# Performance work log

Hardware: AMD Instinct MI355X
Metric: run time of the kernel (lower is better)

Reference implementation:

```python
import jax, jax.numpy as jnp
import numpy as np

N_BUS = 2000
BATCH = 512
N_EDGES = 3072000
SN_MVA = 100.0
ALPHA = 0.9
PHYS_SCALE = 0.02
DEG2RAD = np.pi / 180.0


def setup_inputs() -> dict:
    key = jax.random.key(0)
    ks = jax.random.split(key, 13)
    N = BATCH * N_BUS
    return {
        "y_pred": jax.random.normal(ks[0], (BATCH, N_BUS * 2), jnp.float32),
        "y_true": jax.random.normal(ks[1], (BATCH, N_BUS * 2), jnp.float32),
        "x_input": jax.random.normal(ks[2], (N, 7), jnp.float32),
        "edge_index": jax.random.randint(ks[3], (2, N_EDGES), 0, N),
        "edge_attr": jax.random.normal(ks[4], (N_EDGES, 4), jnp.float32),
        "x_mean": jax.random.normal(ks[5], (N_BUS, 7), jnp.float32),
        "x_std": jax.random.uniform(ks[6], (N_BUS, 7), jnp.float32, 0.5, 1.5),
        "y_mean": jax.random.normal(ks[7], (N_BUS, 2), jnp.float32),
        "y_std": jax.random.uniform(ks[8], (N_BUS, 2), jnp.float32, 0.5, 1.5),
        "edge_mean": jax.random.normal(ks[9], (4,), jnp.float32),
        "edge_std": jax.random.uniform(ks[10], (4,), jnp.float32, 0.5, 1.5),
        "load_bus_mask": jax.random.bernoulli(ks[11], 0.8, (N_BUS,)),
        "bus_shunt_pu": jax.random.normal(ks[12], (N_BUS, 2), jnp.float32) * 0.01,
    }


def reference(y_pred, y_true, x_input, edge_index, edge_attr,
              x_mean, x_std, y_mean, y_std, edge_mean, edge_std,
              load_bus_mask, bus_shunt_pu):
    B, n = BATCH, N_BUS
    N = B * n
    # --- MSE in denormalised target space ---
    yp = y_pred.reshape(B, n, 2) * y_std + y_mean   # [B, n, 2] (Vm, Va_deg)
    yt = y_true.reshape(B, n, 2) * y_std + y_mean
    mse = jnp.mean((yp - yt) ** 2)
    # --- denormalise node features ---
    x_pq = (x_input.reshape(B, n, 7)[:, :, :2] * x_std[:, :2] + x_mean[:, :2])
    x_pq = x_pq.reshape(N, 2) / SN_MVA              # per-unit P, Q demand
    x_phys = jnp.concatenate([yp.reshape(N, 2), x_pq], axis=-1)  # [N,4] Vm,Va,P,Q
    edge_pu = edge_attr * edge_std + edge_mean      # [E,4] Gs,Bs,Gm,Bm
    # --- per-edge power-flow message (flow='target_to_source': i=row0, j=row1) ---
    src, dst = edge_index[0], edge_index[1]
    xi = x_phys[src]
    xj = x_phys[dst]
    vm_i, va_i = xi[:, 0], xi[:, 1] * DEG2RAD
    vm_j, va_j = xj[:, 0], xj[:, 1] * DEG2RAD
    e_i, f_i = vm_i * jnp.cos(va_i), vm_i * jnp.sin(va_i)
    e_j, f_j = vm_j * jnp.cos(va_j), vm_j * jnp.sin(va_j)
    Gs, Bs, Gm, Bm = edge_pu[:, 0], edge_pu[:, 1], edge_pu[:, 2], edge_pu[:, 3]
    I_re = Gs * e_i - Bs * f_i + Gm * e_j - Bm * f_j
    I_im = Gs * f_i + Bs * e_i + Gm * f_j + Bm * e_j
    Pji = -(e_i * I_re + f_i * I_im)
    Qji = -(f_i * I_re - e_i * I_im)
    msg = jnp.stack([Pji, Qji], axis=-1)            # [E,2]
    # --- scatter-add aggregation into source nodes ---
    agg = jax.ops.segment_sum(msg, src, num_segments=N)  # [N,2]
    # --- KCL residual per node ---
    vm_sq = x_phys[:, 0] ** 2
    shunt = jnp.tile(bus_shunt_pu, (B, 1))          # [N,2]
    dP = -agg[:, 0] + x_phys[:, 2] + vm_sq * shunt[:, 0]
    dQ = -agg[:, 1] + x_phys[:, 3] - vm_sq * shunt[:, 1]
    sq = dP ** 2 + dQ ** 2                          # [N]
    w = jnp.tile(load_bus_mask, B).astype(sq.dtype)
    phys = jnp.sum(sq * w) / jnp.sum(w)             # masked mean
    return ALPHA * mse + (1.0 - ALPHA) * PHYS_SCALE * phys
```

## Files before the change

kernel.cpp:

```cpp
#include <hip/hip_runtime.h>
#include <hip/hip_bf16.h>
#include <hip/hip_fp16.h>

#define N_BUS   2000
#define BATCH   512
#define NNODES  (BATCH * N_BUS)
#define NEDGES  3072000

constexpr float SN_INV     = 0.01f;
constexpr float ALPHA_C    = 0.9f;
constexpr float PHYS_SCALE = 0.02f;
constexpr float DEG2RAD_C  = 0.017453292519943295f;

typedef float v4f __attribute__((ext_vector_type(4)));

__device__ __forceinline__ void atomic_pk_add_h2(__half2* addr, float P, float Q) {
    __half2 v = __floats2half2_rn(P, Q);
#if __has_builtin(__builtin_amdgcn_global_atomic_fadd_v2f16)
    typedef _Float16 v2h __attribute__((ext_vector_type(2)));
    __builtin_amdgcn_global_atomic_fadd_v2f16(
        (__attribute__((address_space(1))) v2h*)(void*)addr,
        *reinterpret_cast<v2h*>(&v));
#else
    unsafeAtomicAdd(addr, v);
#endif
}

__device__ __forceinline__ float wave_reduce(float v) {
    #pragma unroll
    for (int off = 32; off > 0; off >>= 1) v += __shfl_down(v, off, 64);
    return v;
}

__global__ __launch_bounds__(256) void node_prep(
    const float* __restrict__ y_pred, const float* __restrict__ y_true,
    const float* __restrict__ x_input,
    const float* __restrict__ x_mean, const float* __restrict__ x_std,
    const float* __restrict__ y_mean, const float* __restrict__ y_std,
    const float* __restrict__ shunt,
    __half2* __restrict__ ef, float2* __restrict__ base,
    __half2* __restrict__ agg, float* __restrict__ acc)
{
    int node = blockIdx.x * blockDim.x + threadIdx.x;
    int i = node % N_BUS;
    float2 ys = *reinterpret_cast<const float2*>(y_std  + (size_t)i*2);
    float2 ym = *reinterpret_cast<const float2*>(y_mean + (size_t)i*2);
    float2 pr = *reinterpret_cast<const float2*>(y_pred + (size_t)node*2);
    float2 tr = *reinterpret_cast<const float2*>(y_true + (size_t)node*2);
    float yp0 = fmaf(pr.x, ys.x, ym.x), yp1 = fmaf(pr.y, ys.y, ym.y);
    float yt0 = fmaf(tr.x, ys.x, ym.x), yt1 = fmaf(tr.y, ys.y, ym.y);
    float d0 = yp0 - yt0, d1 = yp1 - yt1;
    float msep = d0*d0 + d1*d1;

    float s, c;
    __sincosf(yp1 * DEG2RAD_C, &s, &c);
    ef[node] = __floats2half2_rn(yp0 * c, yp0 * s);

    float xi0 = x_input[(size_t)node*7 + 0];
    float xi1 = x_input[(size_t)node*7 + 1];
    float p = fmaf(xi0, x_std[i*7 + 0], x_mean[i*7 + 0]) * SN_INV;
    float q = fmaf(xi1, x_std[i*7 + 1], x_mean[i*7 + 1]) * SN_INV;
    float vm2 = yp0 * yp0;
    float2 sh = *reinterpret_cast<const float2*>(shunt + (size_t)i*2);
    base[node] = make_float2(fmaf(vm2, sh.x, p), fmaf(-vm2, sh.y, q));
    agg[node]  = __floats2half2_rn(0.0f, 0.0f);

    __shared__ float red[4];
    float v = wave_reduce(msep);
    int lane = threadIdx.x & 63, wid = threadIdx.x >> 6;
    if (lane == 0) red[wid] = v;
    __syncthreads();
    if (threadIdx.x == 0)
        unsafeAtomicAdd(acc + 0, red[0] + red[1] + red[2] + red[3]);
}

__global__ __launch_bounds__(256) void edge_kernel(
    const int* __restrict__ eidx, const float* __restrict__ eattr,
    const float* __restrict__ e_mean, const float* __restrict__ e_std,
    const __half2* __restrict__ ef, __half2* __restrict__ agg)
{
    int e = blockIdx.x * blockDim.x + threadIdx.x;
    int s = __builtin_nontemporal_load(eidx + e);
    int d = __builtin_nontemporal_load(eidx + NEDGES + e);
    const v4f* eav = reinterpret_cast<const v4f*>(eattr) + e;
    v4f ea = __builtin_nontemporal_load(eav);
    float Gs = fmaf(ea.x, e_std[0], e_mean[0]);
    float Bs = fmaf(ea.y, e_std[1], e_mean[1]);
    float Gm = fmaf(ea.z, e_std[2], e_mean[2]);
    float Bm = fmaf(ea.w, e_std[3], e_mean[3]);
    float2 fi = __half22float2(ef[s]);
    float2 fj = __half22float2(ef[d]);
    float e_i = fi.x, f_i = fi.y;
    float e_j = fj.x, f_j = fj.y;
    float I_re = Gs*e_i - Bs*f_i + Gm*e_j - Bm*f_j;
    float I_im = Gs*f_i + Bs*e_i + Gm*f_j + Bm*e_j;
    float Pji = -(e_i*I_re + f_i*I_im);
    float Qji = -(f_i*I_re - e_i*I_im);
    atomic_pk_add_h2(agg + s, Pji, Qji);
}

__global__ __launch_bounds__(256) void node_final(
    const float2* __restrict__ base, const __half2* __restrict__ agg,
    const int* __restrict__ mask, float* __restrict__ acc)
{
    int node = blockIdx.x * blockDim.x + threadIdx.x;
    int i = node % N_BUS;
    float2 bs = base[node];
    float2 ag = __half22float2(agg[node]);
    float dP = bs.x - ag.x;
    float dQ = bs.y - ag.y;
    float w  = (mask[i] != 0) ? 1.0f : 0.0f;
    float sqw = (dP*dP + dQ*dQ) * w;

    __shared__ float red0[4], red1[4];
    float v0 = wave_reduce(sqw);
    float v1 = wave_reduce(w);
    int lane = threadIdx.x & 63, wid = threadIdx.x >> 6;
    if (lane == 0) { red0[wid] = v0; red1[wid] = v1; }
    __syncthreads();
    if (threadIdx.x == 0) {
        unsafeAtomicAdd(acc + 1, red0[0] + red0[1] + red0[2] + red0[3]);
        unsafeAtomicAdd(acc + 2, red1[0] + red1[1] + red1[2] + red1[3]);
    }
}

__global__ void finalize_kernel(const float* __restrict__ acc, float* __restrict__ out) {
    if (threadIdx.x == 0 && blockIdx.x == 0) {
        float mse  = acc[0] / (float)(NNODES * 2);
        float phys = acc[1] / acc[2];
        out[0] = ALPHA_C * mse + (1.0f - ALPHA_C) * PHYS_SCALE * phys;
    }
}

extern "C" void kernel_launch(void* const* d_in, const int* in_sizes, int n_in,
                              void* d_out, int out_size, void* d_ws, size_t ws_size,
                              hipStream_t stream) {
    const float* y_pred    = (const float*)d_in[0];
    const float* y_true    = (const float*)d_in[1];
    const float* x_input   = (const float*)d_in[2];
    const int*   edge_idx  = (const int*)  d_in[3];
    const float* edge_attr = (const float*)d_in[4];
    const float* x_mean    = (const float*)d_in[5];
    const float* x_std     = (const float*)d_in[6];
    const float* y_mean    = (const float*)d_in[7];
    const float* y_std     = (const float*)d_in[8];
    const float* edge_mean = (const float*)d_in[9];
    const float* edge_std  = (const float*)d_in[10];
    const int*   load_mask = (const int*)  d_in[11];
    const float* shunt     = (const float*)d_in[12];

    float2*  base = (float2*)d_ws;
    __half2* agg  = (__half2*)(base + NNODES);
    __half2* ef   = agg + NNODES;
    float*   acc  = (float*)(ef + NNODES);

    (void)hipMemsetAsync(acc, 0, 16, stream);

    dim3 blk(256);
    node_prep<<<dim3(NNODES / 256), blk, 0, stream>>>(
        y_pred, y_true, x_input, x_mean, x_std, y_mean, y_std, shunt,
        ef, base, agg, acc);
    edge_kernel<<<dim3(NEDGES / 256), blk, 0, stream>>>(
        edge_idx, edge_attr, edge_mean, edge_std, ef, agg);
    node_final<<<dim3(NNODES / 256), blk, 0, stream>>>(
        base, agg, load_mask, acc);
    finalize_kernel<<<1, 64, 0, stream>>>(acc, (float*)d_out);
}
```

Measured before the change: 443.8 us.

## Drop base buffer, vectorize node kernels, fuse finalize via last-block counter

Moves the P/Q demand and shunt computation from node_prep into node_final, recomputing Vm^2 from the stored fp16 e/f pair, so the float2 base array is no longer written and reread. Both node kernels now handle four nodes per thread with 128-bit loads and stores. The separate finalize kernel is removed by having the last block, detected via an atomic counter, compute the output. Recomputing Vm^2 from fp16 values adds some rounding error in the physics term.

```diff
diff --git a/kernel.cpp b/kernel.cpp
--- a/kernel.cpp
+++ b/kernel.cpp
@@ -34,36 +34,44 @@
 
 __global__ __launch_bounds__(256) void node_prep(
     const float* __restrict__ y_pred, const float* __restrict__ y_true,
-    const float* __restrict__ x_input,
-    const float* __restrict__ x_mean, const float* __restrict__ x_std,
     const float* __restrict__ y_mean, const float* __restrict__ y_std,
-    const float* __restrict__ shunt,
-    __half2* __restrict__ ef, float2* __restrict__ base,
-    __half2* __restrict__ agg, float* __restrict__ acc)
+    __half2* __restrict__ ef, __half2* __restrict__ agg, float* __restrict__ acc)
 {
-    int node = blockIdx.x * blockDim.x + threadIdx.x;
-    int i = node % N_BUS;
-    float2 ys = *reinterpret_cast<const float2*>(y_std  + (size_t)i*2);
-    float2 ym = *reinterpret_cast<const float2*>(y_mean + (size_t)i*2);
-    float2 pr = *reinterpret_cast<const float2*>(y_pred + (size_t)node*2);
-    float2 tr = *reinterpret_cast<const float2*>(y_true + (size_t)node*2);
-    float yp0 = fmaf(pr.x, ys.x, ym.x), yp1 = fmaf(pr.y, ys.y, ym.y);
-    float yt0 = fmaf(tr.x, ys.x, ym.x), yt1 = fmaf(tr.y, ys.y, ym.y);
-    float d0 = yp0 - yt0, d1 = yp1 - yt1;
-    float msep = d0*d0 + d1*d1;
+    int t = blockIdx.x * blockDim.x + threadIdx.x;
+    int n0 = t * 4;
+    int i0 = n0 % N_BUS;
+    float4 pr0 = reinterpret_cast<const float4*>(y_pred + (size_t)n0*2)[0];
+    float4 pr1 = reinterpret_cast<const float4*>(y_pred + (size_t)n0*2)[1];
+    float4 tr0 = reinterpret_cast<const float4*>(y_true + (size_t)n0*2)[0];
+    float4 tr1 = reinterpret_cast<const float4*>(y_true + (size_t)n0*2)[1];
+    float4 ys0 = reinterpret_cast<const float4*>(y_std  + (size_t)i0*2)[0];
+    float4 ys1 = reinterpret_cast<const float4*>(y_std  + (size_t)i0*2)[1];
+    float4 ym0 = reinterpret_cast<const float4*>(y_mean + (size_t)i0*2)[0];
+    float4 ym1 = reinterpret_cast<const float4*>(y_mean + (size_t)i0*2)[1];
 
+    float d, msep = 0.0f;
+    d = (pr0.x - tr0.x) * ys0.x; msep = fmaf(d, d, msep);
+    d = (pr0.y - tr0.y) * ys0.y; msep = fmaf(d, d, msep);
+    d = (pr0.z - tr0.z) * ys0.z; msep = fmaf(d, d, msep);
+    d = (pr0.w - tr0.w) * ys0.w; msep = fmaf(d, d, msep);
+    d = (pr1.x - tr1.x) * ys1.x; msep = fmaf(d, d, msep);
+    d = (pr1.y - tr1.y) * ys1.y; msep = fmaf(d, d, msep);
+    d = (pr1.z - tr1.z) * ys1.z; msep = fmaf(d, d, msep);
+    d = (pr1.w - tr1.w) * ys1.w; msep = fmaf(d, d, msep);
+
+    float vmA = fmaf(pr0.x, ys0.x, ym0.x), vaA = fmaf(pr0.y, ys0.y, ym0.y);
+    float vmB = fmaf(pr0.z, ys0.z, ym0.z), vaB = fmaf(pr0.w, ys0.w, ym0.w);
+    float vmC = fmaf(pr1.x, ys1.x, ym1.x), vaC = fmaf(pr1.y, ys1.y, ym1.y);
+    float vmD = fmaf(pr1.z, ys1.z, ym1.z), vaD = fmaf(pr1.w, ys1.w, ym1.w);
     float s, c;
-    __sincosf(yp1 * DEG2RAD_C, &s, &c);
-    ef[node] = __floats2half2_rn(yp0 * c, yp0 * s);
-
-    float xi0 = x_input[(size_t)node*7 + 0];
-    float xi1 = x_input[(size_t)node*7 + 1];
-    float p = fmaf(xi0, x_std[i*7 + 0], x_mean[i*7 + 0]) * SN_INV;
-    float q = fmaf(xi1, x_std[i*7 + 1], x_mean[i*7 + 1]) * SN_INV;
-    float vm2 = yp0 * yp0;
-    float2 sh = *reinterpret_cast<const float2*>(shunt + (size_t)i*2);
-    base[node] = make_float2(fmaf(vm2, sh.x, p), fmaf(-vm2, sh.y, q));
-    agg[node]  = __floats2half2_rn(0.0f, 0.0f);
+    __sincosf(vaA * DEG2RAD_C, &s, &c); __half2 eA = __floats2half2_rn(vmA*c, vmA*s);
+    __sincosf(vaB * DEG2RAD_C, &s, &c); __half2 eB = __floats2half2_rn(vmB*c, vmB*s);
+    __sincosf(vaC * DEG2RAD_C, &s, &c); __half2 eC = __floats2half2_rn(vmC*c, vmC*s);
+    __sincosf(vaD * DEG2RAD_C, &s, &c); __half2 eD = __floats2half2_rn(vmD*c, vmD*s);
+    *reinterpret_cast<uint4*>(ef + n0) = make_uint4(
+        *reinterpret_cast<unsigned*>(&eA), *reinterpret_cast<unsigned*>(&eB),
+        *reinterpret_cast<unsigned*>(&eC), *reinterpret_cast<unsigned*>(&eD));
+    *reinterpret_cast<uint4*>(agg + n0) = make_uint4(0u, 0u, 0u, 0u);
 
     __shared__ float red[4];
     float v = wave_reduce(msep);
@@ -99,36 +107,62 @@
     atomic_pk_add_h2(agg + s, Pji, Qji);
 }
 
+__device__ __forceinline__ void node_term(
+    unsigned efb, unsigned agb, float shP, float shQ, int m, long n, int i,
+    const float* __restrict__ x_input, const float* __restrict__ x_mean,
+    const float* __restrict__ x_std, float& sqw, float& wsum)
+{
+    float2 efk = __half22float2(*reinterpret_cast<__half2*>(&efb));
+    float2 agk = __half22float2(*reinterpret_cast<__half2*>(&agb));
+    float vm2 = fmaf(efk.x, efk.x, efk.y * efk.y);
+    float p = fmaf(x_input[n*7 + 0], x_std[i*7 + 0], x_mean[i*7 + 0]) * SN_INV;
+    float q = fmaf(x_input[n*7 + 1], x_std[i*7 + 1], x_mean[i*7 + 1]) * SN_INV;
+    float dP = fmaf(vm2, shP, p) - agk.x;
+    float dQ = fmaf(-vm2, shQ, q) - agk.y;
+    float w = m ? 1.0f : 0.0f;
+    sqw = fmaf(dP*dP + dQ*dQ, w, sqw);
+    wsum += w;
+}
+
 __global__ __launch_bounds__(256) void node_final(
-    const float2* __restrict__ base, const __half2* __restrict__ agg,
-    const int* __restrict__ mask, float* __restrict__ acc)
+    const float* __restrict__ x_input,
+    const float* __restrict__ x_mean, const float* __restrict__ x_std,
+    const float* __restrict__ shunt, const int* __restrict__ mask,
+    const __half2* __restrict__ ef, const __half2* __restrict__ agg,
+    float* __restrict__ acc, float* __restrict__ out)
 {
-    int node = blockIdx.x * blockDim.x + threadIdx.x;
-    int i = node % N_BUS;
-    float2 bs = base[node];
-    float2 ag = __half22float2(agg[node]);
-    float dP = bs.x - ag.x;
-    float dQ = bs.y - ag.y;
-    float w  = (mask[i] != 0) ? 1.0f : 0.0f;
-    float sqw = (dP*dP + dQ*dQ) * w;
+    int t = blockIdx.x * blockDim.x + threadIdx.x;
+    int n0 = t * 4;
+    int i0 = n0 % N_BUS;
+    uint4 efu = *reinterpret_cast<const uint4*>(ef + n0);
+    uint4 agu = *reinterpret_cast<const uint4*>(agg + n0);
+    float4 sh0 = reinterpret_cast<const float4*>(shunt + (size_t)i0*2)[0];
+    float4 sh1 = reinterpret_cast<const float4*>(shunt + (size_t)i0*2)[1];
+    int4  mk  = *reinterpret_cast<const int4*>(mask + i0);
+
+    float sqw = 0.0f, wsum = 0.0f;
+    node_term(efu.x, agu.x, sh0.x, sh0.y, mk.x, (long)n0+0, i0+0, x_input, x_mean, x_std, sqw, wsum);
+    node_term(efu.y, agu.y, sh0.z, sh0.w, mk.y, (long)n0+1, i0+1, x_input, x_mean, x_std, sqw, wsum);
+    node_term(efu.z, agu.z, sh1.x, sh1.y, mk.z, (long)n0+2, i0+2, x_input, x_mean, x_std, sqw, wsum);
+    node_term(efu.w, agu.w, sh1.z, sh1.w, mk.w, (long)n0+3, i0+3, x_input, x_mean, x_std, sqw, wsum);
 
     __shared__ float red0[4], red1[4];
     float v0 = wave_reduce(sqw);
-    float v1 = wave_reduce(w);
+    float v1 = wave_reduce(wsum);
     int lane = threadIdx.x & 63, wid = threadIdx.x >> 6;
     if (lane == 0) { red0[wid] = v0; red1[wid] = v1; }
     __syncthreads();
     if (threadIdx.x == 0) {
         unsafeAtomicAdd(acc + 1, red0[0] + red0[1] + red0[2] + red0[3]);
         unsafeAtomicAdd(acc + 2, red1[0] + red1[1] + red1[2] + red1[3]);
-    }
-}
-
-__global__ void finalize_kernel(const float* __restrict__ acc, float* __restrict__ out) {
-    if (threadIdx.x == 0 && blockIdx.x == 0) {
-        float mse  = acc[0] / (float)(NNODES * 2);
-        float phys = acc[1] / acc[2];
-        out[0] = ALPHA_C * mse + (1.0f - ALPHA_C) * PHYS_SCALE * phys;
+        __threadfence();
+        unsigned prev = atomicAdd(reinterpret_cast<unsigned*>(acc + 3), 1u);
+        if (prev == gridDim.x - 1) {
+            float mse = unsafeAtomicAdd(acc + 0, 0.0f) * (1.0f / (2.0f * NNODES));
+            float sq  = unsafeAtomicAdd(acc + 1, 0.0f);
+            float ww  = unsafeAtomicAdd(acc + 2, 0.0f);
+            out[0] = ALPHA_C * mse + (1.0f - ALPHA_C) * PHYS_SCALE * (sq / ww);
+        }
     }
 }
 
@@ -149,20 +183,17 @@
     const int*   load_mask = (const int*)  d_in[11];
     const float* shunt     = (const float*)d_in[12];
 
-    float2*  base = (float2*)d_ws;
-    __half2* agg  = (__half2*)(base + NNODES);
-    __half2* ef   = agg + NNODES;
-    float*   acc  = (float*)(ef + NNODES);
+    __half2* agg = (__half2*)d_ws;
+    __half2* ef  = agg + NNODES;
+    float*   acc = (float*)(ef + NNODES);
 
     (void)hipMemsetAsync(acc, 0, 16, stream);
 
     dim3 blk(256);
-    node_prep<<<dim3(NNODES / 256), blk, 0, stream>>>(
-        y_pred, y_true, x_input, x_mean, x_std, y_mean, y_std, shunt,
-        ef, base, agg, acc);
+    node_prep<<<dim3(NNODES / 1024), blk, 0, stream>>>(
+        y_pred, y_true, y_mean, y_std, ef, agg, acc);
     edge_kernel<<<dim3(NEDGES / 256), blk, 0, stream>>>(
         edge_idx, edge_attr, edge_mean, edge_std, ef, agg);
-    node_final<<<dim3(NNODES / 256), blk, 0, stream>>>(
-        base, agg, load_mask, acc);
-    finalize_kernel<<<1, 64, 0, stream>>>(acc, (float*)d_out);
+    node_final<<<dim3(NNODES / 1024), blk, 0, stream>>>(
+        x_input, x_mean, x_std, shunt, load_mask, ef, agg, acc, (float*)d_out);
 }
```

New measurement: 357.1 us. 1.24x faster.
